# Kernel optimization log

Hardware: AMD Instinct MI355X
Metric: run time of the kernel (lower is better)

## Reference

```python
import jax, jax.numpy as jnp
import numpy as np

N = 2048        # rows of input (nodes / samples)
D_IN = 1024     # input_dim
D_OUT = 8192    # output_dim == number of rows/cols of sparse adj
E = 131072      # nnz of adj (avg degree 16 over D_OUT)


def setup_inputs() -> dict:
    key = jax.random.key(0)
    k0, k1, k2, k3, k4 = jax.random.split(key, 5)
    inp = jax.random.normal(k0, (N, D_IN), dtype=jnp.float32)
    # kaiming_uniform_ on [D_IN, D_OUT]: bound = sqrt(6 / fan_in)
    bound = float(np.sqrt(6.0 / D_IN))
    weight = jax.random.uniform(k1, (D_IN, D_OUT), dtype=jnp.float32,
                                minval=-bound, maxval=bound)
    bias = jnp.zeros((D_OUT,), dtype=jnp.float32)
    adj_rows = jax.random.randint(k2, (E,), 0, D_OUT, dtype=jnp.int64)
    adj_cols = jax.random.randint(k3, (E,), 0, D_OUT, dtype=jnp.int64)
    adj_vals = jax.random.uniform(k4, (E,), dtype=jnp.float32)
    return {"input": inp, "weight": weight, "bias": bias,
            "adj_rows": adj_rows, "adj_cols": adj_cols, "adj_vals": adj_vals}


def reference(input, weight, bias, adj_rows, adj_cols, adj_vals):
    # support = input @ W                      -> [N, D_OUT]
    support = jnp.matmul(input, weight)
    # torch.sparse.mm(adj, support.T).T == (adj @ support^T)^T,
    # with adj sparse COO [D_OUT, D_OUT]: result[r, :] += val_e * support[:, col_e]
    support_t = support.T                      # [D_OUT, N]
    msgs = adj_vals[:, None] * support_t[adj_cols]          # [E, N]
    agg = jax.ops.segment_sum(msgs, adj_rows, num_segments=D_OUT)  # [D_OUT, N]
    return agg.T + bias                        # [N, D_OUT]
```

## Files before the change

### kernel.cpp

```cpp
#include <hip/hip_runtime.h>
#include <hip/hip_bf16.h>


#define N_ROWS 2048
#define D_IN   1024
#define D_OUT  8192

typedef __attribute__((ext_vector_type(8))) short bf16x8;
typedef __attribute__((ext_vector_type(4))) float f32x4;
typedef __attribute__((ext_vector_type(2))) float f32x2;

__device__ __forceinline__ float bf2f(unsigned short u) {
    union { unsigned int i; float f; } x; x.i = ((unsigned int)u) << 16; return x.f;
}
__device__ __forceinline__ unsigned short f2bf(float f) {
    union { unsigned int i; float f; } x; x.f = f;
    unsigned int r = x.i + 0x7FFFu + ((x.i >> 16) & 1u);
    return (unsigned short)(r >> 16);
}

__device__ __forceinline__ void async_load16(const void* g, void* l) {
    __builtin_amdgcn_global_load_lds(
        (const __attribute__((address_space(1))) void*)g,
        (__attribute__((address_space(3))) void*)l,
        16, 0, 0);
}

__global__ __launch_bounds__(256) void transpose_convert(
    const float* __restrict__ w, unsigned short* __restrict__ wt)
{
    __shared__ float tile[64][65];
    const int bx = blockIdx.x;
    const int by = blockIdx.y;
    const int t  = threadIdx.x;
    #pragma unroll
    for (int pass = 0; pass < 4; ++pass) {
        const int item = pass * 256 + t;
        const int r  = item >> 4;
        const int c4 = item & 15;
        const float4 v = *(const float4*)&w[(size_t)(by * 64 + r) * D_OUT + bx * 64 + c4 * 4];
        tile[r][c4 * 4 + 0] = v.x; tile[r][c4 * 4 + 1] = v.y;
        tile[r][c4 * 4 + 2] = v.z; tile[r][c4 * 4 + 3] = v.w;
    }
    __syncthreads();
    #pragma unroll
    for (int pass = 0; pass < 4; ++pass) {
        const int item = pass * 256 + t;
        const int rr  = item >> 4;
        const int cc4 = item & 15;
        ushort4 o;
        o.x = f2bf(tile[cc4 * 4 + 0][rr]);
        o.y = f2bf(tile[cc4 * 4 + 1][rr]);
        o.z = f2bf(tile[cc4 * 4 + 2][rr]);
        o.w = f2bf(tile[cc4 * 4 + 3][rr]);
        *(ushort4*)&wt[(size_t)(bx * 64 + rr) * D_IN + by * 64 + cc4 * 4] = o;
    }
}

__global__ __launch_bounds__(256) void convert_input(
    const float* __restrict__ in, unsigned short* __restrict__ out)
{
    const int i = (blockIdx.x * 256 + threadIdx.x) * 4;
    const float4 v = *(const float4*)(in + i);
    ushort4 o; o.x = f2bf(v.x); o.y = f2bf(v.y); o.z = f2bf(v.z); o.w = f2bf(v.w);
    *(ushort4*)(out + i) = o;
}

__global__ void count_rows(const int* __restrict__ rows, int* counts, int E) {
    int e = blockIdx.x * blockDim.x + threadIdx.x;
    if (e < E) atomicAdd(&counts[rows[e]], 1);
}

__global__ __launch_bounds__(1024) void scan_8192(
    const int* __restrict__ counts, int* __restrict__ offsets)
{
    __shared__ int part[1024];
    const int t = threadIdx.x;
    int loc[8];
    int s = 0;
    #pragma unroll
    for (int j = 0; j < 8; ++j) { loc[j] = s; s += counts[t * 8 + j]; }
    part[t] = s;
    __syncthreads();
    for (int off = 1; off < 1024; off <<= 1) {
        int v = (t >= off) ? part[t - off] : 0;
        __syncthreads();
        part[t] += v;
        __syncthreads();
    }
    const int base = (t == 0) ? 0 : part[t - 1];
    #pragma unroll
    for (int j = 0; j < 8; ++j) offsets[t * 8 + j] = base + loc[j];
    if (t == 1023) offsets[8192] = part[1023];
}

__global__ void fill_csr(const int* __restrict__ rows, const int* __restrict__ cols,
                         const float* __restrict__ vals, const int* __restrict__ offsets,
                         int* cursors, int2* __restrict__ csr_cv, int E) {
    int e = blockIdx.x * blockDim.x + threadIdx.x;
    if (e < E) {
        int r = rows[e];
        int pos = atomicAdd(&cursors[r], 1);
        int2 cv; cv.x = cols[e]; cv.y = __float_as_int(vals[e]);
        csr_cv[offsets[r] + pos] = cv;
    }
}

__global__ __launch_bounds__(256, 8) void aggregate_rows(
    const unsigned short* __restrict__ wtb,
    const int* __restrict__ offsets,
    const int2* __restrict__ csr_cv,
    unsigned short* __restrict__ wpt)
{
    const int wave = threadIdx.x >> 6;
    const int lane = threadIdx.x & 63;
    const int r    = blockIdx.x * 2 + (wave >> 1);
    const int k0   = (wave & 1) * 512 + lane * 8;

    const int beg = offsets[r], end = offsets[r + 1];
    f32x2 acc[4];
    #pragma unroll
    for (int q = 0; q < 4; ++q) acc[q] = (f32x2){0.f, 0.f};

    const unsigned short* wb = wtb + k0;
    int i = beg;
    for (; i + 4 <= end; i += 4) {
        int2 cv[4]; bf16x8 g[4];
        #pragma unroll
        for (int j = 0; j < 4; ++j) cv[j] = csr_cv[i + j];
        #pragma unroll
        for (int j = 0; j < 4; ++j)
            g[j] = *(const bf16x8*)(wb + (size_t)cv[j].x * D_IN);
        #pragma unroll
        for (int j = 0; j < 4; ++j) {
            const float v = __int_as_float(cv[j].y);
            const f32x2 vv = (f32x2){v, v};
            union { bf16x8 s; unsigned int d[4]; } u; u.s = g[j];
            #pragma unroll
            for (int q = 0; q < 4; ++q) {
                union { unsigned int i; float f; } lo, hi;
                lo.i = u.d[q] << 16; hi.i = u.d[q] & 0xffff0000u;
                acc[q] += vv * (f32x2){lo.f, hi.f};
            }
        }
    }
    for (; i < end; ++i) {
        const int2 cv = csr_cv[i];
        const float v = __int_as_float(cv.y);
        const f32x2 vv = (f32x2){v, v};
        union { bf16x8 s; unsigned int d[4]; } u;
        u.s = *(const bf16x8*)(wb + (size_t)cv.x * D_IN);
        #pragma unroll
        for (int q = 0; q < 4; ++q) {
            union { unsigned int i; float f; } lo, hi;
            lo.i = u.d[q] << 16; hi.i = u.d[q] & 0xffff0000u;
            acc[q] += vv * (f32x2){lo.f, hi.f};
        }
    }

    union { bf16x8 s; unsigned short h[8]; } o;
    #pragma unroll
    for (int q = 0; q < 4; ++q) {
        o.h[2 * q]     = f2bf(acc[q][0]);
        o.h[2 * q + 1] = f2bf(acc[q][1]);
    }
    *(bf16x8*)(wpt + (size_t)r * D_IN + k0) = o.s;
}

#define PHASE_MFMA(MI0)                                                         \
    {                                                                           \
        __builtin_amdgcn_sched_barrier(0);                                      \
        __builtin_amdgcn_s_barrier();                                           \
        asm volatile("s_waitcnt lgkmcnt(0)" ::: "memory");                      \
        __builtin_amdgcn_sched_barrier(0);                                      \
        __builtin_amdgcn_s_setprio(1);                                          \
        _Pragma("unroll")                                                       \
        for (int ni = 0; ni < 4; ++ni)                                          \
            acc[MI0][ni]     = __builtin_amdgcn_mfma_f32_16x16x32_bf16(         \
                a00, bfr[0][ni], acc[MI0][ni], 0, 0, 0);                        \
        _Pragma("unroll")                                                       \
        for (int ni = 0; ni < 4; ++ni)                                          \
            acc[MI0 + 1][ni] = __builtin_amdgcn_mfma_f32_16x16x32_bf16(         \
                a10, bfr[0][ni], acc[MI0 + 1][ni], 0, 0, 0);                    \
        _Pragma("unroll")                                                       \
        for (int ni = 0; ni < 4; ++ni)                                          \
            acc[MI0][ni]     = __builtin_amdgcn_mfma_f32_16x16x32_bf16(         \
                a01, bfr[1][ni], acc[MI0][ni], 0, 0, 0);                        \
        _Pragma("unroll")                                                       \
        for (int ni = 0; ni < 4; ++ni)                                          \
            acc[MI0 + 1][ni] = __builtin_amdgcn_mfma_f32_16x16x32_bf16(         \
                a11, bfr[1][ni], acc[MI0 + 1][ni], 0, 0, 0);                    \
        __builtin_amdgcn_s_setprio(0);                                          \
    }

#define READ_A(MI0)                                                             \
    bf16x8 a00 = *(const bf16x8*)(Ab + rowA + (MI0)     * 1024 + x0 * 8);       \
    bf16x8 a01 = *(const bf16x8*)(Ab + rowA + (MI0)     * 1024 + x1 * 8);       \
    bf16x8 a10 = *(const bf16x8*)(Ab + rowA + (MI0 + 1) * 1024 + x0 * 8);       \
    bf16x8 a11 = *(const bf16x8*)(Ab + rowA + (MI0 + 1) * 1024 + x1 * 8);

__global__ __launch_bounds__(512, 2) void gemm_bt_bias(
    const unsigned short* __restrict__ A,
    const unsigned short* __restrict__ B,
    const float*  __restrict__ bias,
    float* __restrict__ C)
{
    __shared__ unsigned short lds[65536];

    const int tid  = threadIdx.x;
    const int wave = tid >> 6;
    const int lane = tid & 63;
    const int q    = lane >> 4;
    const int l16  = lane & 15;
    const int wr   = wave >> 2;
    const int wc   = wave & 3;

    const int bc = blockIdx.x;
    const int br = blockIdx.y;

    const int srow = tid >> 3;
    const int lc   = (tid & 7) ^ (srow & 7);
    const char* Asrc = (const char*)A + ((size_t)(br * 256) + srow) * (D_IN * 2) + lc * 16;
    const char* Bsrc = (const char*)B + ((size_t)(bc * 256) + srow) * (D_IN * 2) + lc * 16;
    char* ldsc = (char*)lds;

    const int x0   = q ^ (l16 & 7);
    const int x1   = x0 ^ 4;
    const int rowA = (wr * 128 + l16) * 64;
    const int rowB = (wc * 64  + l16) * 64;

    f32x4 acc[8][4];
    #pragma unroll
    for (int i = 0; i < 8; ++i)
        #pragma unroll
        for (int j = 0; j < 4; ++j)
            acc[i][j] = (f32x4){0.f, 0.f, 0.f, 0.f};

    #pragma unroll
    for (int j = 0; j < 4; ++j)
        async_load16(Asrc + (size_t)j * 64 * (D_IN * 2), ldsc + j * 8192 + tid * 16);
    #pragma unroll
    for (int j = 0; j < 4; ++j)
        async_load16(Bsrc + (size_t)j * 64 * (D_IN * 2), ldsc + 32768 + j * 8192 + tid * 16);

    for (int kt = 0; kt < D_IN / 64; ++kt) {
        const int cur = kt & 1;
        const unsigned short* Ab = lds + cur * 32768;
        const unsigned short* Bb = Ab + 16384;
        char* dstA = ldsc + (cur ^ 1) * 65536 + tid * 16;
        char* dstB = dstA + 32768;
        const char* srcA = Asrc + (size_t)(kt + 1) * 128;
        const char* srcB = Bsrc + (size_t)(kt + 1) * 128;
        const bool pf = (kt + 1 < D_IN / 64);

        asm volatile("s_waitcnt vmcnt(0)" ::: "memory");
        __builtin_amdgcn_s_barrier();
        if (pf) {
            async_load16(srcA,                            dstA);
            async_load16(srcA + (size_t)64  * (D_IN * 2), dstA + 8192);
            async_load16(srcA + (size_t)128 * (D_IN * 2), dstA + 16384);
            async_load16(srcA + (size_t)192 * (D_IN * 2), dstA + 24576);
        }
        bf16x8 bfr[2][4];
        #pragma unroll
        for (int ni = 0; ni < 4; ++ni) {
            bfr[0][ni] = *(const bf16x8*)(Bb + rowB + ni * 1024 + x0 * 8);
            bfr[1][ni] = *(const bf16x8*)(Bb + rowB + ni * 1024 + x1 * 8);
        }
        {
            READ_A(0)
            PHASE_MFMA(0)
        }

        {
            if (pf) {
                async_load16(srcB,                            dstB);
                async_load16(srcB + (size_t)64  * (D_IN * 2), dstB + 8192);
                async_load16(srcB + (size_t)128 * (D_IN * 2), dstB + 16384);
                async_load16(srcB + (size_t)192 * (D_IN * 2), dstB + 24576);
            }
            READ_A(2)
            PHASE_MFMA(2)
        }

        {
            READ_A(4)
            PHASE_MFMA(4)
        }

        {
            READ_A(6)
            PHASE_MFMA(6)
        }
    }

    #pragma unroll
    for (int ni = 0; ni < 4; ++ni) {
        const int col = bc * 256 + wc * 64 + ni * 16 + l16;
        const float bv = bias[col];
        #pragma unroll
        for (int mi = 0; mi < 8; ++mi) {
            const int row0 = br * 256 + wr * 128 + mi * 16 + q * 4;
            #pragma unroll
            for (int r = 0; r < 4; ++r)
                C[(size_t)(row0 + r) * D_OUT + col] = acc[mi][ni][r] + bv;
        }
    }
}

extern "C" void kernel_launch(void* const* d_in, const int* in_sizes, int n_in,
                              void* d_out, int out_size, void* d_ws, size_t ws_size,
                              hipStream_t stream) {
    (void)n_in; (void)out_size; (void)ws_size;
    const float* input    = (const float*)d_in[0];
    const float* weight   = (const float*)d_in[1];
    const float* bias     = (const float*)d_in[2];
    const int*   adj_rows = (const int*)d_in[3];
    const int*   adj_cols = (const int*)d_in[4];
    const float* adj_vals = (const float*)d_in[5];
    const int E = in_sizes[3];

    char* ws = (char*)d_ws;
    unsigned short* wtb = (unsigned short*)ws;
    unsigned short* wpt = (unsigned short*)(ws + (size_t)16 * 1024 * 1024);
    unsigned short* abf = (unsigned short*)(ws + (size_t)32 * 1024 * 1024);
    int*   counts   = (int*)(ws + (size_t)36 * 1024 * 1024);
    int*   cursors  = counts + D_OUT;
    int*   offsets  = cursors + D_OUT;
    int2*  csr_cv   = (int2*)(offsets + (D_OUT + 4));

    hipMemsetAsync(counts, 0, 2 * D_OUT * sizeof(int), stream);
    transpose_convert<<<dim3(D_OUT / 64, D_IN / 64), 256, 0, stream>>>(weight, wtb);
    convert_input<<<(N_ROWS * D_IN) / 1024, 256, 0, stream>>>(input, abf);
    count_rows<<<(E + 255) / 256, 256, 0, stream>>>(adj_rows, counts, E);
    scan_8192<<<1, 1024, 0, stream>>>(counts, offsets);
    fill_csr<<<(E + 255) / 256, 256, 0, stream>>>(adj_rows, adj_cols, adj_vals,
                                                  offsets, cursors, csr_cv, E);
    aggregate_rows<<<dim3(D_OUT / 2), 256, 0, stream>>>(
        wtb, offsets, csr_cv, wpt);
    gemm_bt_bias<<<dim3(D_OUT / 256, N_ROWS / 256), 512, 0, stream>>>(
        abf, wpt, bias, (float*)d_out);
}
```

Baseline: 190.3 us.

## Software-pipeline LDS fragment reads and drop per-phase barriers in GEMM loop

Restructures the bf16 GEMM main loop so A fragments are double-buffered in registers and loaded one MFMA phase ahead, and next-tile A/B fragments are read right after a single end-of-tile barrier. This removes the barrier and lgkmcnt wait that preceded every MFMA phase, keeping one synchronization per k-tile. It aims to overlap LDS read latency with MFMA execution, at the cost of more live registers, which may pressure occupancy at the 512x2 launch bound.

Measured after the change: 189.8 us. Within noise of the previous version (-0.3%).

```diff
diff --git a/kernel.cpp b/kernel.cpp
--- a/kernel.cpp
+++ b/kernel.cpp
@@ -167,37 +167,40 @@
     *(bf16x8*)(wpt + (size_t)r * D_IN + k0) = o.s;
 }
 
-#define PHASE_MFMA(MI0)                                                         \
-    {                                                                           \
-        __builtin_amdgcn_sched_barrier(0);                                      \
-        __builtin_amdgcn_s_barrier();                                           \
-        asm volatile("s_waitcnt lgkmcnt(0)" ::: "memory");                      \
-        __builtin_amdgcn_sched_barrier(0);                                      \
-        __builtin_amdgcn_s_setprio(1);                                          \
-        _Pragma("unroll")                                                       \
-        for (int ni = 0; ni < 4; ++ni)                                          \
-            acc[MI0][ni]     = __builtin_amdgcn_mfma_f32_16x16x32_bf16(         \
-                a00, bfr[0][ni], acc[MI0][ni], 0, 0, 0);                        \
-        _Pragma("unroll")                                                       \
-        for (int ni = 0; ni < 4; ++ni)                                          \
-            acc[MI0 + 1][ni] = __builtin_amdgcn_mfma_f32_16x16x32_bf16(         \
-                a10, bfr[0][ni], acc[MI0 + 1][ni], 0, 0, 0);                    \
-        _Pragma("unroll")                                                       \
-        for (int ni = 0; ni < 4; ++ni)                                          \
-            acc[MI0][ni]     = __builtin_amdgcn_mfma_f32_16x16x32_bf16(         \
-                a01, bfr[1][ni], acc[MI0][ni], 0, 0, 0);                        \
-        _Pragma("unroll")                                                       \
-        for (int ni = 0; ni < 4; ++ni)                                          \
-            acc[MI0 + 1][ni] = __builtin_amdgcn_mfma_f32_16x16x32_bf16(         \
-                a11, bfr[1][ni], acc[MI0 + 1][ni], 0, 0, 0);                    \
-        __builtin_amdgcn_s_setprio(0);                                          \
-    }
-
-#define READ_A(MI0)                                                             \
-    bf16x8 a00 = *(const bf16x8*)(Ab + rowA + (MI0)     * 1024 + x0 * 8);       \
-    bf16x8 a01 = *(const bf16x8*)(Ab + rowA + (MI0)     * 1024 + x1 * 8);       \
-    bf16x8 a10 = *(const bf16x8*)(Ab + rowA + (MI0 + 1) * 1024 + x0 * 8);       \
-    bf16x8 a11 = *(const bf16x8*)(Ab + rowA + (MI0 + 1) * 1024 + x1 * 8);
+struct QuadFrags { bf16x8 a00, a01, a10, a11; };
+
+#define READQ(Q, BASE, MI0)                                                     \
+    (Q).a00 = *(const bf16x8*)((BASE) + rowA + (MI0)     * 1024 + x0 * 8);      \
+    (Q).a01 = *(const bf16x8*)((BASE) + rowA + (MI0)     * 1024 + x1 * 8);      \
+    (Q).a10 = *(const bf16x8*)((BASE) + rowA + (MI0 + 1) * 1024 + x0 * 8);      \
+    (Q).a11 = *(const bf16x8*)((BASE) + rowA + (MI0 + 1) * 1024 + x1 * 8);
+
+#define READ_BFR(BASE)                                                          \
+    _Pragma("unroll")                                                           \
+    for (int ni = 0; ni < 4; ++ni) {                                            \
+        bfr[0][ni] = *(const bf16x8*)((BASE) + rowB + ni * 1024 + x0 * 8);      \
+        bfr[1][ni] = *(const bf16x8*)((BASE) + rowB + ni * 1024 + x1 * 8);      \
+    }
+
+#define MFMA_Q(Q, MI0)                                                          \
+    __builtin_amdgcn_s_setprio(1);                                              \
+    _Pragma("unroll")                                                           \
+    for (int ni = 0; ni < 4; ++ni)                                              \
+        acc[MI0][ni]     = __builtin_amdgcn_mfma_f32_16x16x32_bf16(             \
+            (Q).a00, bfr[0][ni], acc[MI0][ni], 0, 0, 0);                        \
+    _Pragma("unroll")                                                           \
+    for (int ni = 0; ni < 4; ++ni)                                              \
+        acc[MI0 + 1][ni] = __builtin_amdgcn_mfma_f32_16x16x32_bf16(             \
+            (Q).a10, bfr[0][ni], acc[MI0 + 1][ni], 0, 0, 0);                    \
+    _Pragma("unroll")                                                           \
+    for (int ni = 0; ni < 4; ++ni)                                              \
+        acc[MI0][ni]     = __builtin_amdgcn_mfma_f32_16x16x32_bf16(             \
+            (Q).a01, bfr[1][ni], acc[MI0][ni], 0, 0, 0);                        \
+    _Pragma("unroll")                                                           \
+    for (int ni = 0; ni < 4; ++ni)                                              \
+        acc[MI0 + 1][ni] = __builtin_amdgcn_mfma_f32_16x16x32_bf16(             \
+            (Q).a11, bfr[1][ni], acc[MI0 + 1][ni], 0, 0, 0);                    \
+    __builtin_amdgcn_s_setprio(0);
 
 __global__ __launch_bounds__(512, 2) void gemm_bt_bias(
     const unsigned short* __restrict__ A,
@@ -243,54 +246,58 @@
     for (int j = 0; j < 4; ++j)
         async_load16(Bsrc + (size_t)j * 64 * (D_IN * 2), ldsc + 32768 + j * 8192 + tid * 16);
 
+    asm volatile("s_waitcnt vmcnt(0)" ::: "memory");
+    __builtin_amdgcn_s_barrier();
+
+    QuadFrags RA, RB;
+    bf16x8 bfr[2][4];
+    {
+        const unsigned short* Ab = lds;
+        const unsigned short* Bb = lds + 16384;
+        READ_BFR(Bb)
+        READQ(RA, Ab, 0)
+    }
+
     for (int kt = 0; kt < D_IN / 64; ++kt) {
         const int cur = kt & 1;
         const unsigned short* Ab = lds + cur * 32768;
-        const unsigned short* Bb = Ab + 16384;
         char* dstA = ldsc + (cur ^ 1) * 65536 + tid * 16;
         char* dstB = dstA + 32768;
         const char* srcA = Asrc + (size_t)(kt + 1) * 128;
         const char* srcB = Bsrc + (size_t)(kt + 1) * 128;
         const bool pf = (kt + 1 < D_IN / 64);
 
-        asm volatile("s_waitcnt vmcnt(0)" ::: "memory");
-        __builtin_amdgcn_s_barrier();
         if (pf) {
             async_load16(srcA,                            dstA);
             async_load16(srcA + (size_t)64  * (D_IN * 2), dstA + 8192);
             async_load16(srcA + (size_t)128 * (D_IN * 2), dstA + 16384);
             async_load16(srcA + (size_t)192 * (D_IN * 2), dstA + 24576);
         }
-        bf16x8 bfr[2][4];
-        #pragma unroll
-        for (int ni = 0; ni < 4; ++ni) {
-            bfr[0][ni] = *(const bf16x8*)(Bb + rowB + ni * 1024 + x0 * 8);
-            bfr[1][ni] = *(const bf16x8*)(Bb + rowB + ni * 1024 + x1 * 8);
-        }
-        {
-            READ_A(0)
-            PHASE_MFMA(0)
-        }
-
-        {
-            if (pf) {
-                async_load16(srcB,                            dstB);
-                async_load16(srcB + (size_t)64  * (D_IN * 2), dstB + 8192);
-                async_load16(srcB + (size_t)128 * (D_IN * 2), dstB + 16384);
-                async_load16(srcB + (size_t)192 * (D_IN * 2), dstB + 24576);
-            }
-            READ_A(2)
-            PHASE_MFMA(2)
-        }
-
-        {
-            READ_A(4)
-            PHASE_MFMA(4)
-        }
-
-        {
-            READ_A(6)
-            PHASE_MFMA(6)
+        READQ(RB, Ab, 2)
+        MFMA_Q(RA, 0)
+
+        if (pf) {
+            async_load16(srcB,                            dstB);
+            async_load16(srcB + (size_t)64  * (D_IN * 2), dstB + 8192);
+            async_load16(srcB + (size_t)128 * (D_IN * 2), dstB + 16384);
+            async_load16(srcB + (size_t)192 * (D_IN * 2), dstB + 24576);
+        }
+        READQ(RA, Ab, 4)
+        MFMA_Q(RB, 2)
+
+        READQ(RB, Ab, 6)
+        MFMA_Q(RA, 4)
+
+        if (pf) {
+            asm volatile("s_waitcnt vmcnt(0) lgkmcnt(0)" ::: "memory");
+            __builtin_amdgcn_s_barrier();
+            const unsigned short* Abn = lds + (cur ^ 1) * 32768;
+            READQ(RA, Abn, 0)
+            MFMA_Q(RB, 6)
+            const unsigned short* Bbn = Abn + 16384;
+            READ_BFR(Bbn)
+        } else {
+            MFMA_Q(RB, 6)
         }
     }
 
```
